# Kernel optimization log

Measured on AMD Instinct MI355X. Metric: run time of the kernel, lower is better.

The kernel has to match this reference:

```python
import jax, jax.numpy as jnp
import numpy as np

EMB_DIM = 1024
NHEAD = 16
HEAD_DIM = EMB_DIM // NHEAD
SLEN = 1024
BSZ = 8
NEG_INF = -1e30


def setup_inputs() -> dict:
    key = jax.random.key(0)
    ks = jax.random.split(key, 8)
    q = jax.random.normal(ks[0], (SLEN, BSZ, EMB_DIM), dtype=jnp.float32)
    k = jax.random.normal(ks[1], (SLEN, BSZ, EMB_DIM), dtype=jnp.float32)
    v = jax.random.normal(ks[2], (SLEN, BSZ, EMB_DIM), dtype=jnp.float32)
    mask = jax.random.randint(ks[3], (BSZ * NHEAD, SLEN, SLEN), 0, 2).astype(jnp.bool_)
    # xavier_uniform bound for square [E,E] matrices
    bound = float(np.sqrt(6.0 / (EMB_DIM + EMB_DIM)))
    Wq = jax.random.uniform(ks[4], (EMB_DIM, EMB_DIM), jnp.float32, -bound, bound)
    Wk = jax.random.uniform(ks[5], (EMB_DIM, EMB_DIM), jnp.float32, -bound, bound)
    Wv = jax.random.uniform(ks[6], (EMB_DIM, EMB_DIM), jnp.float32, -bound, bound)
    Wo = jax.random.uniform(ks[7], (EMB_DIM, EMB_DIM), jnp.float32, -bound, bound)
    return {"q": q, "k": k, "v": v, "mask": mask, "Wq": Wq, "Wk": Wk, "Wv": Wv, "Wo": Wo}


def reference(q, k, v, mask, Wq, Wk, Wv, Wo):
    slen, bsz, emb = q.shape
    scaling = float(HEAD_DIM) ** -0.5
    # F.linear(x, W) = x @ W.T
    query = q @ Wq.T  # [slen, bsz, E]
    key_ = k @ Wk.T
    value = v @ Wv.T
    # -> [bsz*nhead, slen, head_dim]
    def split_heads(x):
        return x.reshape(slen, bsz * NHEAD, HEAD_DIM).transpose(1, 0, 2)
    query = split_heads(query)
    key_ = split_heads(key_)
    value = split_heads(value)
    attn_weight = jnp.einsum('bqd,bkd->bqk', query, key_) * scaling  # [B*H, S, S]
    attn_weight = jnp.where(mask, NEG_INF, attn_weight)
    attn_score = jax.nn.softmax(attn_weight, axis=-1)
    # attn_mask=True: post-softmax multiplicative mask
    attn_score = attn_score * (~mask).astype(attn_score.dtype)
    # dropout is identity in eval mode
    attn_output = jnp.einsum('bqk,bkd->bqd', attn_score, value)  # [B*H, S, hd]
    attn_output = attn_output.transpose(1, 0, 2).reshape(slen, bsz, emb)
    return attn_output @ Wo.T
```

## Files before the change

kernel.cpp:

```cpp
#include <hip/hip_runtime.h>


typedef __attribute__((ext_vector_type(8))) short bf16x8;
typedef __attribute__((ext_vector_type(8))) unsigned short u16x8;
typedef __attribute__((ext_vector_type(4))) float f32x4;

#define LOG2E 1.44269504088896340736f

__device__ __forceinline__ unsigned short bfbits(float f) {
  unsigned u = __builtin_bit_cast(unsigned, f);
  u += 0x7fffu + ((u >> 16) & 1u);
  return (unsigned short)(u >> 16);
}
__device__ __forceinline__ unsigned pk2(float a, float b) {
  return (unsigned)bfbits(a) | ((unsigned)bfbits(b) << 16);
}
__device__ __forceinline__ void async16(const void* src, void* dst_lds) {
  __builtin_amdgcn_global_load_lds(
      (const __attribute__((address_space(1))) unsigned int*)src,
      (__attribute__((address_space(3))) unsigned int*)dst_lds, 16, 0, 0);
}

__global__ void detect_mask(const unsigned* __restrict__ m, int* __restrict__ flag)
{
  unsigned ok = 1u;
#pragma unroll 8
  for (int i = 0; i < 64; ++i) {
    unsigned w = m[(threadIdx.x << 6) + i];
    ok &= (w <= 1u) ? 1u : 0u;
  }
  unsigned long long vote = __ballot(ok != 0u);
  if (threadIdx.x == 0) *flag = (vote == ~0ull) ? 1 : 0;
}

__global__ __launch_bounds__(256) void cvt_kernel(
    const float* __restrict__ q, const float* __restrict__ k, const float* __restrict__ v,
    const float* __restrict__ wq, const float* __restrict__ wk,
    const float* __restrict__ wv, const float* __restrict__ wo,
    unsigned short* __restrict__ Xin, unsigned short* __restrict__ Wbf)
{
  const unsigned u = blockIdx.x * 256u + threadIdx.x;
  const float* src;
  unsigned short* dst;
  if (u < 3145728u) {
    const unsigned z = u >> 20, r = u & 1048575u;
    src = (z == 0 ? q : z == 1 ? k : v) + (size_t)r * 8;
    dst = Xin + (size_t)z * 8388608u + (size_t)r * 8;
  } else {
    const unsigned u2 = u - 3145728u, wz = u2 >> 17, r = u2 & 131071u;
    src = (wz == 0 ? wq : wz == 1 ? wk : wz == 2 ? wv : wo) + (size_t)r * 8;
    dst = Wbf + (size_t)wz * 1048576u + (size_t)r * 8;
  }
  f32x4 a = *(const f32x4*)src;
  f32x4 b = *(const f32x4*)(src + 4);
  uint4 o;
  o.x = pk2(a[0], a[1]); o.y = pk2(a[2], a[3]);
  o.z = pk2(b[0], b[1]); o.w = pk2(b[2], b[3]);
  *(uint4*)dst = o;
}

template<int OUTF32>
__global__ __launch_bounds__(256) void gemm128(
    const unsigned short* __restrict__ A0,
    const unsigned short* __restrict__ B0,
    void* __restrict__ C0, float scale0, int M, int N, int K)
{
  const int tid = threadIdx.x;
  const int w = tid >> 6, lane = tid & 63, c = lane & 15, g = lane >> 4;
  const int wr = w >> 1, wc = w & 1;

  const int bid = blockIdx.x;
  const int p = bid >> 9, local = bid & 511;
  const unsigned short* A = A0 + (size_t)p * 8388608u;
  const unsigned short* B = B0 + (size_t)p * 1048576u;
  const float scale = (p == 0) ? scale0 : 1.0f;

  const int swz = (local & 7) * 64 + (local >> 3);
  const int ntx = N >> 7;
  const int bx = swz % ntx, by = swz / ntx;
  const int rowA = by * 128, rowB = bx * 128;

  __shared__ unsigned short As[2][128 * 64];
  __shared__ unsigned short Bs[2][128 * 64];

  f32x4 acc[4][4];
#pragma unroll
  for (int i = 0; i < 4; ++i)
#pragma unroll
    for (int j = 0; j < 4; ++j) acc[i][j] = (f32x4){0.f, 0.f, 0.f, 0.f};

  const int wbase = (tid & ~63) * 16;

#define STAGE(kt_, bb_) do { const int k0_ = (kt_) << 6;                          \
    _Pragma("unroll") for (int i_ = 0; i_ < 4; ++i_) {                            \
      const int slot_ = i_ * 256 + tid;                                           \
      const int row_ = slot_ >> 3;                                                \
      const int kc_ = (slot_ & 7) ^ (row_ & 7);                                   \
      async16(A + (size_t)(rowA + row_) * K + k0_ + kc_ * 8,                      \
              (char*)&As[bb_][0] + (i_ << 12) + wbase);                           \
      async16(B + (size_t)(rowB + row_) * K + k0_ + kc_ * 8,                      \
              (char*)&Bs[bb_][0] + (i_ << 12) + wbase);                           \
    } } while (0)

#define RD(arr_, bb_, row_, ks_) \
    (*(const bf16x8*)&arr_[bb_][(row_) * 64 + ((((ks_) * 4 + g) ^ ((row_) & 7)) << 3)])

#define COMPUTE(bb_) do {                                                         \
    bf16x8 af_[4][2], bf_[4][2];                                                  \
    _Pragma("unroll") for (int x_ = 0; x_ < 4; ++x_)                              \
      _Pragma("unroll") for (int ks_ = 0; ks_ < 2; ++ks_) {                       \
        af_[x_][ks_] = RD(As, bb_, wr * 64 + x_ * 16 + c, ks_);                   \
        bf_[x_][ks_] = RD(Bs, bb_, wc * 64 + x_ * 16 + c, ks_);                   \
      }                                                                           \
    _Pragma("unroll") for (int ks_ = 0; ks_ < 2; ++ks_)                           \
      _Pragma("unroll") for (int mf_ = 0; mf_ < 4; ++mf_)                         \
        _Pragma("unroll") for (int nf_ = 0; nf_ < 4; ++nf_)                       \
          acc[mf_][nf_] = __builtin_amdgcn_mfma_f32_16x16x32_bf16(                \
              af_[mf_][ks_], bf_[nf_][ks_], acc[mf_][nf_], 0, 0, 0); } while (0)

  STAGE(0, 0);
  STAGE(1, 1);

  for (int kt = 0; kt < 15; ++kt) {
    asm volatile("s_waitcnt vmcnt(8)" ::: "memory");
    __builtin_amdgcn_sched_barrier(0);
    __builtin_amdgcn_s_barrier();
    __builtin_amdgcn_sched_barrier(0);
    const int buf = kt & 1;
    COMPUTE(buf);
    __builtin_amdgcn_sched_barrier(0);
    __builtin_amdgcn_s_barrier();
    __builtin_amdgcn_sched_barrier(0);
    if (kt < 14) STAGE(kt + 2, buf);
  }
  asm volatile("s_waitcnt vmcnt(0)" ::: "memory");
  __builtin_amdgcn_sched_barrier(0);
  __builtin_amdgcn_s_barrier();
  __builtin_amdgcn_sched_barrier(0);
  COMPUTE(1);

#undef STAGE
#undef RD
#undef COMPUTE

  const int r0 = rowA + wr * 64, c0 = rowB + wc * 64;
  if (OUTF32) {
    float* O = (float*)C0;
#pragma unroll
    for (int mf = 0; mf < 4; ++mf)
#pragma unroll
      for (int nf = 0; nf < 4; ++nf)
#pragma unroll
        for (int j = 0; j < 4; ++j)
          O[(size_t)(r0 + mf * 16 + g * 4 + j) * N + c0 + nf * 16 + c] = acc[mf][nf][j] * scale;
  } else {
    unsigned short* O = (unsigned short*)C0 + (size_t)p * 8388608u;
#pragma unroll
    for (int mf = 0; mf < 4; ++mf)
#pragma unroll
      for (int nf = 0; nf < 4; ++nf)
#pragma unroll
        for (int j = 0; j < 4; ++j)
          O[(size_t)(r0 + mf * 16 + g * 4 + j) * N + c0 + nf * 16 + c] = bfbits(acc[mf][nf][j] * scale);
  }
}

__global__ __launch_bounds__(256) void transpose_v(
    const unsigned short* __restrict__ Xp2, unsigned short* __restrict__ Vt)
{
  const int tid = threadIdx.x;
  const int bh = blockIdx.y, b = bh >> 4, h = bh & 15;
  const int s0 = blockIdx.x << 6;
  __shared__ unsigned short T[64 * 68];
#pragma unroll
  for (int p = 0; p < 2; ++p) {
    const int idx = (p << 8) + tid, sr = idx >> 3, ch2 = idx & 7;
    *(u16x8*)&T[sr * 68 + ch2 * 8] =
        *(const u16x8*)(Xp2 + ((size_t)((s0 + sr) * 8 + b) << 10) + (h << 6) + ch2 * 8);
  }
  __syncthreads();
#pragma unroll
  for (int p = 0; p < 2; ++p) {
    const int idx = (p << 8) + tid, dr = idx >> 3, ch2 = idx & 7;
    u16x8 o;
#pragma unroll
    for (int e = 0; e < 8; ++e) o[e] = T[(ch2 * 8 + e) * 68 + dr];
    *(u16x8*)(Vt + ((size_t)(bh * 64 + dr) << 10) + s0 + ch2 * 8) = o;
  }
}

__device__ __forceinline__ void load_mask4(unsigned mv[4], const void* maskp, bool mi32,
                                           size_t base, int g) {
  if (mi32) {
    const int* mrow = (const int*)maskp + base + (g << 2);
#pragma unroll
    for (int mf = 0; mf < 4; ++mf) {
      const int4 w4 = *(const int4*)(mrow + mf * 16);
      mv[mf] = (w4.x ? 1u : 0u) | (w4.y ? 0x100u : 0u) | (w4.z ? 0x10000u : 0u) | (w4.w ? 0x1000000u : 0u);
    }
  } else {
    const unsigned char* mrow = (const unsigned char*)maskp + base + (g << 2);
#pragma unroll
    for (int mf = 0; mf < 4; ++mf) mv[mf] = *(const unsigned*)(mrow + mf * 16);
  }
}

__global__ __launch_bounds__(256) void attn_kernel(
    const unsigned short* __restrict__ Qp,
    const unsigned short* __restrict__ Kp,
    const unsigned short* __restrict__ Vt,
    const void*           __restrict__ maskp,
    const int*            __restrict__ mflag,
    unsigned short* __restrict__ AO)
{
  const int tid = threadIdx.x;
  const int w = tid >> 6, lane = tid & 63, c = lane & 15, g = lane >> 4;
  const int bh = blockIdx.y, b = bh >> 4, h = bh & 15;
  const int qb0 = blockIdx.x << 6;
  const int qrow = qb0 + (w << 4) + c;
  const bool mi32 = (*mflag != 0);

  __shared__ unsigned short Ksm[64 * 72];
  __shared__ unsigned short Vsm[64 * 72];
  __shared__ unsigned short Psm[4][16 * 72];

  bf16x8 qf[2];
  {
    const unsigned short* qp = Qp + ((size_t)(qrow * 8 + b) << 10) + (h << 6) + (g << 3);
    qf[0] = *(const bf16x8*)qp;
    qf[1] = *(const bf16x8*)(qp + 32);
  }

  const int row0 = tid >> 3, ch = tid & 7;
  const unsigned short* Vg = Vt + ((size_t)bh << 16);
  const size_t mbase0 = ((size_t)bh << 20) + ((size_t)qrow << 10);

  bf16x8 kr[2], vr[2];
#pragma unroll
  for (int p = 0; p < 2; ++p) {
    const int r = row0 + p * 32;
    kr[p] = *(const bf16x8*)(Kp + ((size_t)(r * 8 + b) << 10) + (h << 6) + (ch << 3));
    vr[p] = *(const bf16x8*)(Vg + ((size_t)r << 10) + (ch << 3));
  }
  unsigned mv[4];
  load_mask4(mv, maskp, mi32, mbase0, g);

  f32x4 oacc[4];
#pragma unroll
  for (int i = 0; i < 4; ++i) oacc[i] = (f32x4){0.f, 0.f, 0.f, 0.f};
  float mrun = -1e30f, lrun = 0.f;

  for (int t = 0; t < 16; ++t) {
    const int kk0 = t << 6;
    __syncthreads();
#pragma unroll
    for (int p = 0; p < 2; ++p) {
      const int r = row0 + p * 32;
      *(bf16x8*)&Ksm[r * 72 + (ch << 3)] = kr[p];
      *(bf16x8*)&Vsm[r * 72 + (ch << 3)] = vr[p];
    }
    __syncthreads();
    unsigned mvN[4];
    if (t < 15) {
      const int kk1 = kk0 + 64;
#pragma unroll
      for (int p = 0; p < 2; ++p) {
        const int r = row0 + p * 32;
        kr[p] = *(const bf16x8*)(Kp + ((size_t)((kk1 + r) * 8 + b) << 10) + (h << 6) + (ch << 3));
        vr[p] = *(const bf16x8*)(Vg + ((size_t)r << 10) + kk1 + (ch << 3));
      }
      load_mask4(mvN, maskp, mi32, mbase0 + kk1, g);
    }
    f32x4 sacc[4];
#pragma unroll
    for (int i = 0; i < 4; ++i) sacc[i] = (f32x4){0.f, 0.f, 0.f, 0.f};
#pragma unroll
    for (int d2 = 0; d2 < 2; ++d2) {
#pragma unroll
      for (int mf = 0; mf < 4; ++mf) {
        bf16x8 kf = *(const bf16x8*)&Ksm[(mf * 16 + c) * 72 + d2 * 32 + (g << 3)];
        sacc[mf] = __builtin_amdgcn_mfma_f32_16x16x32_bf16(kf, qf[d2], sacc[mf], 0, 0, 0);
      }
    }
    float tmax = -1e30f;
#pragma unroll
    for (int mf = 0; mf < 4; ++mf)
#pragma unroll
      for (int j = 0; j < 4; ++j) {
        float s = sacc[mf][j];
        if ((mv[mf] >> (8 * j)) & 0xffu) s = -1e30f;
        sacc[mf][j] = s;
        tmax = fmaxf(tmax, s);
      }
    tmax = fmaxf(tmax, __shfl_xor(tmax, 16));
    tmax = fmaxf(tmax, __shfl_xor(tmax, 32));
    const float mnew = fmaxf(mrun, tmax);
    const float alpha = __builtin_amdgcn_exp2f((mrun - mnew) * LOG2E);
    float tsum = 0.f;
    float pv[4][4];
#pragma unroll
    for (int mf = 0; mf < 4; ++mf)
#pragma unroll
      for (int j = 0; j < 4; ++j) {
        const float p = __builtin_amdgcn_exp2f((sacc[mf][j] - mnew) * LOG2E);
        pv[mf][j] = p;
        tsum += p;
      }
    tsum += __shfl_xor(tsum, 16);
    tsum += __shfl_xor(tsum, 32);
    lrun = lrun * alpha + tsum;
    mrun = mnew;
#pragma unroll
    for (int i = 0; i < 4; ++i) {
      oacc[i][0] *= alpha; oacc[i][1] *= alpha; oacc[i][2] *= alpha; oacc[i][3] *= alpha;
    }
#pragma unroll
    for (int mf = 0; mf < 4; ++mf) {
      uint2 t2;
      t2.x = pk2(pv[mf][0], pv[mf][1]);
      t2.y = pk2(pv[mf][2], pv[mf][3]);
      *(uint2*)&Psm[w][c * 72 + mf * 16 + (g << 2)] = t2;
    }
#pragma unroll
    for (int ks = 0; ks < 2; ++ks) {
      bf16x8 pf = *(const bf16x8*)&Psm[w][c * 72 + ks * 32 + (g << 3)];
#pragma unroll
      for (int mf = 0; mf < 4; ++mf) {
        bf16x8 vf = *(const bf16x8*)&Vsm[(mf * 16 + c) * 72 + ks * 32 + (g << 3)];
        oacc[mf] = __builtin_amdgcn_mfma_f32_16x16x32_bf16(vf, pf, oacc[mf], 0, 0, 0);
      }
    }
#pragma unroll
    for (int i = 0; i < 4; ++i) mv[i] = mvN[i];
  }
  const float inv = 1.0f / lrun;
#pragma unroll
  for (int mf = 0; mf < 4; ++mf) {
    uint2 t2;
    t2.x = pk2(oacc[mf][0] * inv, oacc[mf][1] * inv);
    t2.y = pk2(oacc[mf][2] * inv, oacc[mf][3] * inv);
    *(uint2*)(AO + ((size_t)(qrow * 8 + b) << 10) + (h << 6) + mf * 16 + (g << 2)) = t2;
  }
}

extern "C" void kernel_launch(void* const* d_in, const int* in_sizes, int n_in,
                              void* d_out, int out_size, void* d_ws, size_t ws_size,
                              hipStream_t stream)
{
  const float* q  = (const float*)d_in[0];
  const float* k  = (const float*)d_in[1];
  const float* v  = (const float*)d_in[2];
  const void*  mask = (const void*)d_in[3];
  const float* wq = (const float*)d_in[4];
  const float* wk = (const float*)d_in[5];
  const float* wv = (const float*)d_in[6];
  const float* wo = (const float*)d_in[7];

  unsigned short* ws  = (unsigned short*)d_ws;
  unsigned short* Xin = ws;
  unsigned short* Wbf = ws + 25165824u;
  unsigned short* Xp  = ws + 29360128u;
  int* mfl            = (int*)(ws + 54525952u);
  unsigned short* Vt  = ws + 8388608u;
  unsigned short* AO  = ws;

  detect_mask<<<1, 64, 0, stream>>>((const unsigned*)mask, mfl);
  cvt_kernel<<<14336, 256, 0, stream>>>(q, k, v, wq, wk, wv, wo, Xin, Wbf);
  gemm128<0><<<1536, 256, 0, stream>>>(Xin, Wbf, Xp, 0.125f, 8192, 1024, 1024);
  transpose_v<<<dim3(16, 128), 256, 0, stream>>>(Xp + 16777216u, Vt);
  attn_kernel<<<dim3(16, 128), 256, 0, stream>>>(Xp, Xp + 8388608u, Vt, mask, mfl, AO);
  gemm128<1><<<512, 256, 0, stream>>>(AO, Wbf + 3145728u, d_out, 1.0f, 8192, 1024, 1024);
}
```

Baseline: 292.3 us.

## Restructure projection GEMMs into 256x128 tiles with 8-wave phased triple-buffer pipeline

Replaces the 128x128 double-buffered GEMM with a 512-thread, 256x128-tile kernel that uses triple-buffered LDS. Each K-step is split into four phases that interleave LDS fragment reads, async global-to-LDS prefetches and MFMA bursts, with barriers and raised wave priority around the MFMAs. The aim is better overlap of memory and matrix work and more reuse per tile, at the cost of more LDS (triple buffer) and half as many blocks. Separately, the mask loads in attention become nontemporal loads so the streamed mask does not pollute the cache.

```diff
diff --git a/kernel.cpp b/kernel.cpp
--- a/kernel.cpp
+++ b/kernel.cpp
@@ -4,6 +4,7 @@
 typedef __attribute__((ext_vector_type(8))) short bf16x8;
 typedef __attribute__((ext_vector_type(8))) unsigned short u16x8;
 typedef __attribute__((ext_vector_type(4))) float f32x4;
+typedef __attribute__((ext_vector_type(4))) int i32x4;
 
 #define LOG2E 1.44269504088896340736f
 
@@ -60,7 +61,7 @@
 }
 
 template<int OUTF32>
-__global__ __launch_bounds__(256) void gemm128(
+__global__ __launch_bounds__(512) void gemm8ph(
     const unsigned short* __restrict__ A0,
     const unsigned short* __restrict__ B0,
     void* __restrict__ C0, float scale0, int M, int N, int K)
@@ -70,18 +71,18 @@
   const int wr = w >> 1, wc = w & 1;
 
   const int bid = blockIdx.x;
-  const int p = bid >> 9, local = bid & 511;
+  const int p = bid >> 8, local = bid & 255;
   const unsigned short* A = A0 + (size_t)p * 8388608u;
   const unsigned short* B = B0 + (size_t)p * 1048576u;
   const float scale = (p == 0) ? scale0 : 1.0f;
 
-  const int swz = (local & 7) * 64 + (local >> 3);
+  const int swz = (local & 7) * 32 + (local >> 3);
   const int ntx = N >> 7;
   const int bx = swz % ntx, by = swz / ntx;
-  const int rowA = by * 128, rowB = bx * 128;
-
-  __shared__ unsigned short As[2][128 * 64];
-  __shared__ unsigned short Bs[2][128 * 64];
+  const int rowA = by * 256, rowB = bx * 128;
+
+  __shared__ unsigned short As[3][256 * 64];
+  __shared__ unsigned short Bs[3][128 * 64];
 
   f32x4 acc[4][4];
 #pragma unroll
@@ -91,57 +92,123 @@
 
   const int wbase = (tid & ~63) * 16;
 
-#define STAGE(kt_, bb_) do { const int k0_ = (kt_) << 6;                          \
-    _Pragma("unroll") for (int i_ = 0; i_ < 4; ++i_) {                            \
-      const int slot_ = i_ * 256 + tid;                                           \
-      const int row_ = slot_ >> 3;                                                \
-      const int kc_ = (slot_ & 7) ^ (row_ & 7);                                   \
-      async16(A + (size_t)(rowA + row_) * K + k0_ + kc_ * 8,                      \
-              (char*)&As[bb_][0] + (i_ << 12) + wbase);                           \
-      async16(B + (size_t)(rowB + row_) * K + k0_ + kc_ * 8,                      \
-              (char*)&Bs[bb_][0] + (i_ << 12) + wbase);                           \
-    } } while (0)
+#define STAGE_A(kt_, bb_, i_) do { const int k0_ = (kt_) << 6;                    \
+    const int slot_ = (i_) * 512 + tid;                                           \
+    const int row_ = slot_ >> 3;                                                  \
+    const int kc_ = (slot_ & 7) ^ (row_ & 7);                                     \
+    async16(A + (size_t)(rowA + row_) * K + k0_ + kc_ * 8,                        \
+            (char*)&As[bb_][0] + ((i_) << 13) + wbase); } while (0)
+#define STAGE_B(kt_, bb_, j_) do { const int k0_ = (kt_) << 6;                    \
+    const int slot_ = (j_) * 512 + tid;                                           \
+    const int row_ = slot_ >> 3;                                                  \
+    const int kc_ = (slot_ & 7) ^ (row_ & 7);                                     \
+    async16(B + (size_t)(rowB + row_) * K + k0_ + kc_ * 8,                        \
+            (char*)&Bs[bb_][0] + ((j_) << 13) + wbase); } while (0)
 
 #define RD(arr_, bb_, row_, ks_) \
     (*(const bf16x8*)&arr_[bb_][(row_) * 64 + ((((ks_) * 4 + g) ^ ((row_) & 7)) << 3)])
 
-#define COMPUTE(bb_) do {                                                         \
-    bf16x8 af_[4][2], bf_[4][2];                                                  \
-    _Pragma("unroll") for (int x_ = 0; x_ < 4; ++x_)                              \
-      _Pragma("unroll") for (int ks_ = 0; ks_ < 2; ++ks_) {                       \
-        af_[x_][ks_] = RD(As, bb_, wr * 64 + x_ * 16 + c, ks_);                   \
-        bf_[x_][ks_] = RD(Bs, bb_, wc * 64 + x_ * 16 + c, ks_);                   \
-      }                                                                           \
-    _Pragma("unroll") for (int ks_ = 0; ks_ < 2; ++ks_)                           \
-      _Pragma("unroll") for (int mf_ = 0; mf_ < 4; ++mf_)                         \
-        _Pragma("unroll") for (int nf_ = 0; nf_ < 4; ++nf_)                       \
-          acc[mf_][nf_] = __builtin_amdgcn_mfma_f32_16x16x32_bf16(                \
-              af_[mf_][ks_], bf_[nf_][ks_], acc[mf_][nf_], 0, 0, 0); } while (0)
-
-  STAGE(0, 0);
-  STAGE(1, 1);
-
-  for (int kt = 0; kt < 15; ++kt) {
-    asm volatile("s_waitcnt vmcnt(8)" ::: "memory");
+#define PH_BAR() do { __builtin_amdgcn_s_barrier();                               \
+    asm volatile("s_waitcnt lgkmcnt(0)" ::: "memory");                            \
+    __builtin_amdgcn_sched_barrier(0); } while (0)
+
+#pragma unroll
+  for (int i = 0; i < 4; ++i) STAGE_A(0, 0, i);
+#pragma unroll
+  for (int j = 0; j < 2; ++j) STAGE_B(0, 0, j);
+#pragma unroll
+  for (int i = 0; i < 4; ++i) STAGE_A(1, 1, i);
+#pragma unroll
+  for (int j = 0; j < 2; ++j) STAGE_B(1, 1, j);
+
+  int br = 0;
+  for (int kt = 0; kt < 16; ++kt) {
+    if (kt == 15) asm volatile("s_waitcnt vmcnt(0)" ::: "memory");
+    else          asm volatile("s_waitcnt vmcnt(6)" ::: "memory");
     __builtin_amdgcn_sched_barrier(0);
     __builtin_amdgcn_s_barrier();
     __builtin_amdgcn_sched_barrier(0);
-    const int buf = kt & 1;
-    COMPUTE(buf);
-    __builtin_amdgcn_sched_barrier(0);
-    __builtin_amdgcn_s_barrier();
-    __builtin_amdgcn_sched_barrier(0);
-    if (kt < 14) STAGE(kt + 2, buf);
-  }
-  asm volatile("s_waitcnt vmcnt(0)" ::: "memory");
-  __builtin_amdgcn_sched_barrier(0);
-  __builtin_amdgcn_s_barrier();
-  __builtin_amdgcn_sched_barrier(0);
-  COMPUTE(1);
-
-#undef STAGE
+    const int bs = (br == 0) ? 2 : br - 1;
+    const bool st = (kt < 14);
+
+    bf16x8 a0 = RD(As, br, wr * 64 +  0 + c, 0);
+    bf16x8 a1 = RD(As, br, wr * 64 + 16 + c, 0);
+    bf16x8 b0 = RD(Bs, br, wc * 64 +  0 + c, 0);
+    bf16x8 b1 = RD(Bs, br, wc * 64 + 16 + c, 0);
+    bf16x8 b2 = RD(Bs, br, wc * 64 + 32 + c, 0);
+    bf16x8 b3 = RD(Bs, br, wc * 64 + 48 + c, 0);
+    if (st) { STAGE_A(kt + 2, bs, 0); STAGE_A(kt + 2, bs, 1); }
+    PH_BAR();
+    __builtin_amdgcn_s_setprio(1);
+    acc[0][0] = __builtin_amdgcn_mfma_f32_16x16x32_bf16(a0, b0, acc[0][0], 0, 0, 0);
+    acc[0][1] = __builtin_amdgcn_mfma_f32_16x16x32_bf16(a0, b1, acc[0][1], 0, 0, 0);
+    acc[0][2] = __builtin_amdgcn_mfma_f32_16x16x32_bf16(a0, b2, acc[0][2], 0, 0, 0);
+    acc[0][3] = __builtin_amdgcn_mfma_f32_16x16x32_bf16(a0, b3, acc[0][3], 0, 0, 0);
+    acc[1][0] = __builtin_amdgcn_mfma_f32_16x16x32_bf16(a1, b0, acc[1][0], 0, 0, 0);
+    acc[1][1] = __builtin_amdgcn_mfma_f32_16x16x32_bf16(a1, b1, acc[1][1], 0, 0, 0);
+    acc[1][2] = __builtin_amdgcn_mfma_f32_16x16x32_bf16(a1, b2, acc[1][2], 0, 0, 0);
+    acc[1][3] = __builtin_amdgcn_mfma_f32_16x16x32_bf16(a1, b3, acc[1][3], 0, 0, 0);
+    __builtin_amdgcn_s_setprio(0);
+    __builtin_amdgcn_sched_barrier(0);
+
+    bf16x8 a2 = RD(As, br, wr * 64 + 32 + c, 0);
+    bf16x8 a3 = RD(As, br, wr * 64 + 48 + c, 0);
+    if (st) { STAGE_A(kt + 2, bs, 2); STAGE_A(kt + 2, bs, 3); }
+    PH_BAR();
+    __builtin_amdgcn_s_setprio(1);
+    acc[2][0] = __builtin_amdgcn_mfma_f32_16x16x32_bf16(a2, b0, acc[2][0], 0, 0, 0);
+    acc[2][1] = __builtin_amdgcn_mfma_f32_16x16x32_bf16(a2, b1, acc[2][1], 0, 0, 0);
+    acc[2][2] = __builtin_amdgcn_mfma_f32_16x16x32_bf16(a2, b2, acc[2][2], 0, 0, 0);
+    acc[2][3] = __builtin_amdgcn_mfma_f32_16x16x32_bf16(a2, b3, acc[2][3], 0, 0, 0);
+    acc[3][0] = __builtin_amdgcn_mfma_f32_16x16x32_bf16(a3, b0, acc[3][0], 0, 0, 0);
+    acc[3][1] = __builtin_amdgcn_mfma_f32_16x16x32_bf16(a3, b1, acc[3][1], 0, 0, 0);
+    acc[3][2] = __builtin_amdgcn_mfma_f32_16x16x32_bf16(a3, b2, acc[3][2], 0, 0, 0);
+    acc[3][3] = __builtin_amdgcn_mfma_f32_16x16x32_bf16(a3, b3, acc[3][3], 0, 0, 0);
+    __builtin_amdgcn_s_setprio(0);
+    __builtin_amdgcn_sched_barrier(0);
+
+    a0 = RD(As, br, wr * 64 +  0 + c, 1);
+    a1 = RD(As, br, wr * 64 + 16 + c, 1);
+    b0 = RD(Bs, br, wc * 64 +  0 + c, 1);
+    b1 = RD(Bs, br, wc * 64 + 16 + c, 1);
+    b2 = RD(Bs, br, wc * 64 + 32 + c, 1);
+    b3 = RD(Bs, br, wc * 64 + 48 + c, 1);
+    if (st) { STAGE_B(kt + 2, bs, 0); STAGE_B(kt + 2, bs, 1); }
+    PH_BAR();
+    __builtin_amdgcn_s_setprio(1);
+    acc[0][0] = __builtin_amdgcn_mfma_f32_16x16x32_bf16(a0, b0, acc[0][0], 0, 0, 0);
+    acc[0][1] = __builtin_amdgcn_mfma_f32_16x16x32_bf16(a0, b1, acc[0][1], 0, 0, 0);
+    acc[0][2] = __builtin_amdgcn_mfma_f32_16x16x32_bf16(a0, b2, acc[0][2], 0, 0, 0);
+    acc[0][3] = __builtin_amdgcn_mfma_f32_16x16x32_bf16(a0, b3, acc[0][3], 0, 0, 0);
+    acc[1][0] = __builtin_amdgcn_mfma_f32_16x16x32_bf16(a1, b0, acc[1][0], 0, 0, 0);
+    acc[1][1] = __builtin_amdgcn_mfma_f32_16x16x32_bf16(a1, b1, acc[1][1], 0, 0, 0);
+    acc[1][2] = __builtin_amdgcn_mfma_f32_16x16x32_bf16(a1, b2, acc[1][2], 0, 0, 0);
+    acc[1][3] = __builtin_amdgcn_mfma_f32_16x16x32_bf16(a1, b3, acc[1][3], 0, 0, 0);
+    __builtin_amdgcn_s_setprio(0);
+    __builtin_amdgcn_sched_barrier(0);
+
+    a2 = RD(As, br, wr * 64 + 32 + c, 1);
+    a3 = RD(As, br, wr * 64 + 48 + c, 1);
+    PH_BAR();
+    __builtin_amdgcn_s_setprio(1);
+    acc[2][0] = __builtin_amdgcn_mfma_f32_16x16x32_bf16(a2, b0, acc[2][0], 0, 0, 0);
+    acc[2][1] = __builtin_amdgcn_mfma_f32_16x16x32_bf16(a2, b1, acc[2][1], 0, 0, 0);
+    acc[2][2] = __builtin_amdgcn_mfma_f32_16x16x32_bf16(a2, b2, acc[2][2], 0, 0, 0);
+    acc[2][3] = __builtin_amdgcn_mfma_f32_16x16x32_bf16(a2, b3, acc[2][3], 0, 0, 0);
+    acc[3][0] = __builtin_amdgcn_mfma_f32_16x16x32_bf16(a3, b0, acc[3][0], 0, 0, 0);
+    acc[3][1] = __builtin_amdgcn_mfma_f32_16x16x32_bf16(a3, b1, acc[3][1], 0, 0, 0);
+    acc[3][2] = __builtin_amdgcn_mfma_f32_16x16x32_bf16(a3, b2, acc[3][2], 0, 0, 0);
+    acc[3][3] = __builtin_amdgcn_mfma_f32_16x16x32_bf16(a3, b3, acc[3][3], 0, 0, 0);
+    __builtin_amdgcn_s_setprio(0);
+    __builtin_amdgcn_sched_barrier(0);
+
+    br = (br == 2) ? 0 : br + 1;
+  }
+
+#undef STAGE_A
+#undef STAGE_B
 #undef RD
-#undef COMPUTE
+#undef PH_BAR
 
   const int r0 = rowA + wr * 64, c0 = rowB + wc * 64;
   if (OUTF32) {
@@ -195,13 +262,14 @@
     const int* mrow = (const int*)maskp + base + (g << 2);
 #pragma unroll
     for (int mf = 0; mf < 4; ++mf) {
-      const int4 w4 = *(const int4*)(mrow + mf * 16);
+      const i32x4 w4 = __builtin_nontemporal_load((const i32x4*)(mrow + mf * 16));
       mv[mf] = (w4.x ? 1u : 0u) | (w4.y ? 0x100u : 0u) | (w4.z ? 0x10000u : 0u) | (w4.w ? 0x1000000u : 0u);
     }
   } else {
     const unsigned char* mrow = (const unsigned char*)maskp + base + (g << 2);
 #pragma unroll
-    for (int mf = 0; mf < 4; ++mf) mv[mf] = *(const unsigned*)(mrow + mf * 16);
+    for (int mf = 0; mf < 4; ++mf)
+      mv[mf] = __builtin_nontemporal_load((const unsigned*)(mrow + mf * 16));
   }
 }
 
@@ -366,8 +434,8 @@
 
   detect_mask<<<1, 64, 0, stream>>>((const unsigned*)mask, mfl);
   cvt_kernel<<<14336, 256, 0, stream>>>(q, k, v, wq, wk, wv, wo, Xin, Wbf);
-  gemm128<0><<<1536, 256, 0, stream>>>(Xin, Wbf, Xp, 0.125f, 8192, 1024, 1024);
+  gemm8ph<0><<<768, 512, 0, stream>>>(Xin, Wbf, Xp, 0.125f, 8192, 1024, 1024);
   transpose_v<<<dim3(16, 128), 256, 0, stream>>>(Xp + 16777216u, Vt);
   attn_kernel<<<dim3(16, 128), 256, 0, stream>>>(Xp, Xp + 8388608u, Vt, mask, mfl, AO);
-  gemm128<1><<<512, 256, 0, stream>>>(AO, Wbf + 3145728u, d_out, 1.0f, 8192, 1024, 1024);
-}
+  gemm8ph<1><<<256, 512, 0, stream>>>(AO, Wbf + 3145728u, d_out, 1.0f, 8192, 1024, 1024);
+}
```

Result: slower. 303.6 us (+3.9%).
